# Performance work log

Hardware: AMD Instinct MI355X
Metric: run time of the kernel (lower is better)

## Reference

```python
import jax, jax.numpy as jnp
import numpy as np

B, L, D_MODEL = 4, 2048, 1024
D_STATE, D_CONV, EXPAND = 16, 4, 2
D_INNER = EXPAND * D_MODEL
DT_RANK = D_MODEL // 16
EPS = 1e-5


def layernorm(x, g, b):
    mu = jnp.mean(x, axis=-1, keepdims=True)
    var = jnp.mean(jnp.square(x - mu), axis=-1, keepdims=True)
    return (x - mu) * jax.lax.rsqrt(var + EPS) * g + b


def mamba(h, in_proj_w, conv_w, conv_b, x_proj_w, dt_proj_w, dt_proj_b, A_log, Dp, out_proj_w):
    # in projection -> [B, L, 2*D_INNER]
    xz = jnp.einsum('bld,ed->ble', h, in_proj_w)
    xi, z = jnp.split(xz, 2, axis=-1)
    # causal depthwise conv over time: [B, D_INNER, L]
    xc = jnp.transpose(xi, (0, 2, 1))
    xc = jax.lax.conv_general_dilated(
        xc, conv_w, window_strides=(1,), padding=[(D_CONV - 1, 0)],
        dimension_numbers=('NCH', 'OIH', 'NCH'), feature_group_count=D_INNER)
    xc = xc + conv_b[None, :, None]
    xi = jax.nn.silu(jnp.transpose(xc, (0, 2, 1)))  # [B, L, D_INNER]
    # data-dependent SSM params
    x_dbl = jnp.einsum('bld,ed->ble', xi, x_proj_w)  # [B, L, DT_RANK + 2*N]
    dt, Bm, Cm = jnp.split(x_dbl, [DT_RANK, DT_RANK + D_STATE], axis=-1)
    dt = jax.nn.softplus(jnp.einsum('blr,dr->bld', dt, dt_proj_w) + dt_proj_b)  # [B, L, D_INNER]
    A = -jnp.exp(A_log)  # [D_INNER, D_STATE]

    def step(hstate, inp):
        dt_t, B_t, C_t, u_t = inp  # [B,Din], [B,N], [B,N], [B,Din]
        dA = jnp.exp(dt_t[..., None] * A)                   # [B, Din, N]
        dBu = dt_t[..., None] * B_t[:, None, :] * u_t[..., None]
        hstate = dA * hstate + dBu
        y_t = jnp.sum(hstate * C_t[:, None, :], axis=-1)    # [B, Din]
        return hstate, y_t

    h0 = jnp.zeros((B, D_INNER, D_STATE), dtype=h.dtype)
    xs = (jnp.swapaxes(dt, 0, 1), jnp.swapaxes(Bm, 0, 1),
          jnp.swapaxes(Cm, 0, 1), jnp.swapaxes(xi, 0, 1))
    _, ys = jax.lax.scan(step, h0, xs)  # ys: [L, B, D_INNER]
    y = jnp.swapaxes(ys, 0, 1) + Dp * xi
    y = y * jax.nn.silu(z)
    return jnp.einsum('ble,de->bld', y, out_proj_w)


def setup_inputs() -> dict:
    key = jax.random.key(0)
    ks = jax.random.split(key, 16)
    s = 0.02
    inp = {
        'x': jax.random.normal(ks[0], (B, L, D_MODEL), jnp.float32),
        'ln1_g': jnp.ones((D_MODEL,), jnp.float32),
        'ln1_b': jnp.zeros((D_MODEL,), jnp.float32),
        'ln2_g': jnp.ones((D_MODEL,), jnp.float32),
        'ln2_b': jnp.zeros((D_MODEL,), jnp.float32),
        'in_proj_w': jax.random.normal(ks[1], (2 * D_INNER, D_MODEL), jnp.float32) * s,
        'conv_w': jax.random.normal(ks[2], (D_INNER, 1, D_CONV), jnp.float32) * 0.1,
        'conv_b': jnp.zeros((D_INNER,), jnp.float32),
        'x_proj_w': jax.random.normal(ks[3], (DT_RANK + 2 * D_STATE, D_INNER), jnp.float32) * s,
        'dt_proj_w': jax.random.normal(ks[4], (D_INNER, DT_RANK), jnp.float32) * 0.1,
        'dt_proj_b': jnp.full((D_INNER,), -4.0, jnp.float32),
        'A_log': jnp.log(jnp.broadcast_to(jnp.arange(1, D_STATE + 1, dtype=jnp.float32), (D_INNER, D_STATE))),
        'Dp': jnp.ones((D_INNER,), jnp.float32),
        'out_proj_w': jax.random.normal(ks[5], (D_MODEL, D_INNER), jnp.float32) * s,
        'ffn_w1': jax.random.normal(ks[6], (4 * D_MODEL, D_MODEL), jnp.float32) * s,
        'ffn_b1': jnp.zeros((4 * D_MODEL,), jnp.float32),
        'ffn_w2': jax.random.normal(ks[7], (D_MODEL, 4 * D_MODEL), jnp.float32) * s,
        'ffn_b2': jnp.zeros((D_MODEL,), jnp.float32),
    }
    return inp


def reference(x, ln1_g, ln1_b, ln2_g, ln2_b, in_proj_w, conv_w, conv_b, x_proj_w,
              dt_proj_w, dt_proj_b, A_log, Dp, out_proj_w, ffn_w1, ffn_b1, ffn_w2, ffn_b2):
    x = x + mamba(layernorm(x, ln1_g, ln1_b), in_proj_w, conv_w, conv_b,
                  x_proj_w, dt_proj_w, dt_proj_b, A_log, Dp, out_proj_w)
    h2 = layernorm(x, ln2_g, ln2_b)
    ffn = jnp.einsum('bld,fd->blf', h2, ffn_w1) + ffn_b1
    ffn = jnp.einsum('blf,df->bld', jax.nn.relu(ffn), ffn_w2) + ffn_b2
    return x + ffn  # dropout is identity in eval mode
```

## Files before the change

kernel.cpp:

```cpp
#include <hip/hip_runtime.h>

using u16 = unsigned short;
using u32 = unsigned int;

typedef short s16x8 __attribute__((ext_vector_type(8)));
typedef float f32x4 __attribute__((ext_vector_type(4)));

#define DEV static __device__ __forceinline__
#define AS1 __attribute__((address_space(1)))
#define AS3 __attribute__((address_space(3)))

DEV u16 f2bf(float f){
  u32 u = __float_as_uint(f);
  return (u16)((u + 0x7fffu + ((u >> 16) & 1u)) >> 16);
}
DEV float bf2f(u16 h){ return __uint_as_float(((u32)h) << 16); }

DEV void gload_lds16(const u16* g, u16* l){
  __builtin_amdgcn_global_load_lds((const AS1 void*)g, (AS3 void*)l, 16, 0, 0);
}

__global__ __launch_bounds__(256) void cast_w(
    const float* __restrict__ s0, const float* __restrict__ s1,
    const float* __restrict__ s2, const float* __restrict__ s3,
    const float* __restrict__ s4, const float* __restrict__ s5,
    u16* __restrict__ dst)
{
  size_t base = ((size_t)blockIdx.x * 256 + threadIdx.x) * 4;
  if (base >= 15007744u) return;
  const float* src; size_t off;
  if      (base <  4194304u){ src=s0; off=base;           }
  else if (base <  4390912u){ src=s1; off=base- 4194304u; }
  else if (base <  4521984u){ src=s2; off=base- 4390912u; }
  else if (base <  6619136u){ src=s3; off=base- 4521984u; }
  else if (base < 10813440u){ src=s4; off=base- 6619136u; }
  else                      { src=s5; off=base-10813440u; }
  float4 v = *(const float4*)(src + off);
  *(ushort4*)(dst + base) = make_ushort4(f2bf(v.x), f2bf(v.y), f2bf(v.z), f2bf(v.w));
}

__global__ __launch_bounds__(256) void ln_bf16(
    const float* __restrict__ x, const float* __restrict__ g,
    const float* __restrict__ b, u16* __restrict__ o)
{
  int row = blockIdx.x, t = threadIdx.x;
  float4 v = ((const float4*)(x + (size_t)row*1024))[t];
  float s  = v.x+v.y+v.z+v.w;
  float ss = v.x*v.x+v.y*v.y+v.z*v.z+v.w*v.w;
  #pragma unroll
  for (int off=32; off; off>>=1){ s += __shfl_down(s,off); ss += __shfl_down(ss,off); }
  __shared__ float red[8];
  int lane = t & 63, w = t >> 6;
  if (lane==0){ red[w]=s; red[4+w]=ss; }
  __syncthreads();
  float S  = red[0]+red[1]+red[2]+red[3];
  float SS = red[4]+red[5]+red[6]+red[7];
  float mu = S * (1.f/1024.f);
  float var = SS * (1.f/1024.f) - mu*mu;
  float rs = rsqrtf(var + 1e-5f);
  float4 gg = ((const float4*)g)[t], bb = ((const float4*)b)[t];
  ((ushort4*)o)[(size_t)row*256 + t] = make_ushort4(
    f2bf((v.x-mu)*rs*gg.x + bb.x), f2bf((v.y-mu)*rs*gg.y + bb.y),
    f2bf((v.z-mu)*rs*gg.z + bb.z), f2bf((v.w-mu)*rs*gg.w + bb.w));
}

__global__ __launch_bounds__(256) void conv_silu(
    const u16* __restrict__ xi, const float* __restrict__ cw,
    const float* __restrict__ cb, u16* __restrict__ ob)
{
  int idx = blockIdx.x*256 + threadIdx.x;
  int d4 = (idx & 511) << 2;
  int l  = (idx >> 9) & 2047;
  int b  = idx >> 20;
  float4 w0 = ((const float4*)cw)[d4+0];
  float4 w1 = ((const float4*)cw)[d4+1];
  float4 w2 = ((const float4*)cw)[d4+2];
  float4 w3 = ((const float4*)cw)[d4+3];
  float4 bb = *(const float4*)(cb + d4);
  float a0=bb.x, a1=bb.y, a2=bb.z, a3=bb.w;
  size_t rowbase = ((size_t)b*2048 + l)*2048 + d4;
  #pragma unroll
  for (int j=0;j<4;j++){
    int ls = l - 3 + j;
    if (ls >= 0){
      ushort4 xv = *(const ushort4*)(xi + rowbase + (size_t)(j-3)*2048);
      a0 += (&w0.x)[j]*bf2f(xv.x);
      a1 += (&w1.x)[j]*bf2f(xv.y);
      a2 += (&w2.x)[j]*bf2f(xv.z);
      a3 += (&w3.x)[j]*bf2f(xv.w);
    }
  }
  ushort4 o;
  o.x = f2bf(a0/(1.f+__expf(-a0)));
  o.y = f2bf(a1/(1.f+__expf(-a1)));
  o.z = f2bf(a2/(1.f+__expf(-a2)));
  o.w = f2bf(a3/(1.f+__expf(-a3)));
  *(ushort4*)(ob + rowbase) = o;
}

__global__ __launch_bounds__(256) void xred(
    const float* __restrict__ xp, float* __restrict__ xd, u16* __restrict__ dr)
{
  int i = blockIdx.x*256 + threadIdx.x;
  float v = xp[i] + xp[786432 + i] + xp[2*786432 + i] + xp[3*786432 + i];
  xd[i] = v;
  int row = i / 96, col = i - row*96;
  if (col < 64) dr[(size_t)row*64 + col] = f2bf(v);
}


__global__ __launch_bounds__(256) void scan_a(
    const u16* __restrict__ dtq, const u16* __restrict__ u,
    const float* __restrict__ xdbl, const float* __restrict__ alog,
    float* __restrict__ hend, float* __restrict__ sdt)
{
  int d = blockIdx.x*256 + threadIdx.x;
  int b = blockIdx.y, s = blockIdx.z, l0 = s*64;
  __shared__ float sB[64][16];
  for (int i = threadIdx.x; i < 1024; i += 256){
    int row = i >> 4, c = i & 15;
    sB[row][c] = xdbl[((size_t)(b*2048 + l0 + row))*96 + 64 + c];
  }
  float afn[16];
  #pragma unroll
  for (int n=0;n<16;n++) afn[n] = -__expf(alog[d*16+n]);
  __syncthreads();
  float h[16];
  #pragma unroll
  for (int n=0;n<16;n++) h[n] = 0.f;
  float sum_dt = 0.f;
  size_t base = ((size_t)b*2048 + l0)*2048 + d;
  for (int t=0;t<64;t++){
    float dtv = bf2f(dtq[base]);
    float uv  = bf2f(u[base]);
    sum_dt += dtv;
    float dtu = dtv*uv;
    #pragma unroll
    for (int n=0;n<16;n++)
      h[n] = __expf(dtv*afn[n])*h[n] + dtu*sB[t][n];
    base += 2048;
  }
  sdt[(b*32+s)*2048 + d] = sum_dt;
  size_t hb = ((size_t)(b*32+s)*16)*2048 + d;
  #pragma unroll
  for (int n=0;n<16;n++) hend[hb + (size_t)n*2048] = h[n];
}

__global__ __launch_bounds__(256) void scan_b(
    float* __restrict__ hend, const float* __restrict__ sdt,
    const float* __restrict__ alog)
{
  int g = blockIdx.x*256 + threadIdx.x;
  int d = g & 2047, n = (g >> 11) & 15, b = g >> 15;
  float An = -__expf(alog[d*16+n]);
  float h = 0.f;
  for (int s=0;s<32;s++){
    size_t hi = ((size_t)((b*32+s)*16) + n)*2048 + d;
    float he = hend[hi];
    hend[hi] = h;
    h = he + h*__expf(An * sdt[(b*32+s)*2048 + d]);
  }
}

__global__ __launch_bounds__(256) void scan_c(
    const u16* __restrict__ dtq, const u16* __restrict__ u,
    const u16* __restrict__ zb, const float* __restrict__ xdbl,
    const float* __restrict__ alog, const float* __restrict__ dp,
    const float* __restrict__ hstart, u16* __restrict__ yg)
{
  int d = blockIdx.x*256 + threadIdx.x;
  int b = blockIdx.y, s = blockIdx.z, l0 = s*64;
  __shared__ float sB[64][16], sC[64][16];
  for (int i = threadIdx.x; i < 1024; i += 256){
    int row = i >> 4, c = i & 15;
    size_t xb = ((size_t)(b*2048 + l0 + row))*96 + 64;
    sB[row][c] = xdbl[xb + c];
    sC[row][c] = xdbl[xb + 16 + c];
  }
  float afn[16];
  #pragma unroll
  for (int n=0;n<16;n++) afn[n] = -__expf(alog[d*16+n]);
  __syncthreads();
  float h[16];
  size_t hb = ((size_t)((b*32+s)*16))*2048 + d;
  #pragma unroll
  for (int n=0;n<16;n++) h[n] = hstart[hb + (size_t)n*2048];
  float Dpd = dp[d];
  size_t base = ((size_t)b*2048 + l0)*2048 + d;
  for (int t=0;t<64;t++){
    float dtv = bf2f(dtq[base]);
    float uv  = bf2f(u[base]);
    float dtu = dtv*uv;
    float y = 0.f;
    #pragma unroll
    for (int n=0;n<16;n++){
      h[n] = __expf(dtv*afn[n])*h[n] + dtu*sB[t][n];
      y += h[n]*sC[t][n];
    }
    float zv = bf2f(zb[base]);
    float yv = (y + Dpd*uv) * (zv / (1.f + __expf(-zv)));
    yg[base] = f2bf(yv);
    base += 2048;
  }
}

template<int EPI>
__global__ __launch_bounds__(256) void gemm_bt(
    const u16* __restrict__ A, const u16* __restrict__ W,
    int M, int N, int K, int Nreal,
    float* __restrict__ F0, const float* __restrict__ C0,
    const float* __restrict__ C1, u16* __restrict__ OB, u16* __restrict__ OB2)
{
  __shared__ __attribute__((aligned(16))) u16 sA[128*32];
  __shared__ __attribute__((aligned(16))) u16 sB[128*32];
  const int tid  = threadIdx.x;
  const int lane = tid & 63;
  const int wid  = tid >> 6;
  const int wr = wid >> 1, wc = wid & 1;
  const int bm = blockIdx.y * 128, bn = blockIdx.x * 128;

  const int kchunk = K / (int)gridDim.z;
  const int k0 = (int)blockIdx.z * kchunk, k1 = k0 + kchunk;

  f32x4 acc[4][4];
  #pragma unroll
  for (int m=0;m<4;m++)
    #pragma unroll
    for (int nn=0;nn<4;nn++) acc[m][nn] = (f32x4){0.f,0.f,0.f,0.f};

  const int c0 = tid,        r0a = c0 >> 2, cc0 = c0 & 3;
  const int c1 = tid + 256,  r1a = c1 >> 2, cc1 = c1 & 3;
  int wrow0 = bn + r0a; if (wrow0 > Nreal-1) wrow0 = Nreal-1;
  int wrow1 = bn + r1a; if (wrow1 > Nreal-1) wrow1 = Nreal-1;

  const int frow = lane & 15;
  const int ksel = lane >> 4;

  for (int kt = k0; kt < k1; kt += 32){
    gload_lds16(A + (size_t)(bm + r0a)*K + kt + cc0*8, &sA[c0*8]);
    gload_lds16(A + (size_t)(bm + r1a)*K + kt + cc1*8, &sA[c1*8]);
    gload_lds16(W + (size_t)wrow0*K + kt + cc0*8, &sB[c0*8]);
    gload_lds16(W + (size_t)wrow1*K + kt + cc1*8, &sB[c1*8]);
    __syncthreads();
    s16x8 af[4], bfr[4];
    #pragma unroll
    for (int m=0;m<4;m++)
      af[m] = *(const s16x8*)&sA[(wr*64 + m*16 + frow)*32 + ksel*8];
    #pragma unroll
    for (int nn=0;nn<4;nn++)
      bfr[nn] = *(const s16x8*)&sB[(wc*64 + nn*16 + frow)*32 + ksel*8];
    #pragma unroll
    for (int m=0;m<4;m++)
      #pragma unroll
      for (int nn=0;nn<4;nn++)
        acc[m][nn] = __builtin_amdgcn_mfma_f32_16x16x32_bf16(af[m], bfr[nn], acc[m][nn], 0, 0, 0);
    __syncthreads();
  }

  const int crow0 = (lane >> 4) * 4;
  const int ccol  = lane & 15;
  #pragma unroll
  for (int m=0;m<4;m++){
    #pragma unroll
    for (int nn=0;nn<4;nn++){
      #pragma unroll
      for (int j=0;j<4;j++){
        int grow = bm + wr*64 + m*16 + crow0 + j;
        int gcol = bn + wc*64 + nn*16 + ccol;
        float v = acc[m][nn][j];
        if constexpr (EPI==0){
          if (gcol < 2048) OB2[(size_t)grow*2048 + gcol] = f2bf(v);
          else             OB[(size_t)grow*2048 + (gcol-2048)] = f2bf(v);
        } else if constexpr (EPI==1){
          if (gcol < Nreal)
            F0[((size_t)blockIdx.z*M + grow)*Nreal + gcol] = v;
        } else if constexpr (EPI==2){
          v += C0[gcol];
          v = (v > 20.f) ? v : log1pf(__expf(v));
          OB[(size_t)grow*N + gcol] = f2bf(v);
        } else if constexpr (EPI==3){
          F0[(size_t)grow*N + gcol] = v + C1[(size_t)grow*N + gcol];
        } else if constexpr (EPI==4){
          v += C0[gcol]; v = fmaxf(v, 0.f);
          OB[(size_t)grow*N + gcol] = f2bf(v);
        } else {
          F0[(size_t)grow*N + gcol] = v + C0[gcol] + C1[(size_t)grow*N + gcol];
        }
      }
    }
  }
}

extern "C" void kernel_launch(void* const* d_in, const int* in_sizes, int n_in,
                              void* d_out, int out_size, void* d_ws, size_t ws_size,
                              hipStream_t stream)
{
  const float* X    = (const float*)d_in[0];
  const float* LN1G = (const float*)d_in[1];
  const float* LN1B = (const float*)d_in[2];
  const float* LN2G = (const float*)d_in[3];
  const float* LN2B = (const float*)d_in[4];
  const float* INW  = (const float*)d_in[5];
  const float* CONVW= (const float*)d_in[6];
  const float* CONVB= (const float*)d_in[7];
  const float* XPW  = (const float*)d_in[8];
  const float* DTW  = (const float*)d_in[9];
  const float* DTBIA= (const float*)d_in[10];
  const float* ALOG = (const float*)d_in[11];
  const float* DP   = (const float*)d_in[12];
  const float* OUTW = (const float*)d_in[13];
  const float* W1   = (const float*)d_in[14];
  const float* B1   = (const float*)d_in[15];
  const float* W2   = (const float*)d_in[16];
  const float* B2   = (const float*)d_in[17];

  char* ws = (char*)d_ws;
  u16* WB   = (u16*)ws;
  u16* bIN  = WB;
  u16* bXP  = WB + 4194304;
  u16* bDT  = WB + 4390912;
  u16* bOUT = WB + 4521984;
  u16* bW1  = WB + 6619136;
  u16* bW2  = WB + 10813440;
  u16*   H1    = (u16*)(ws + 30015488);
  float* HEND  = (float*)(ws + 30015488);
  u16*   ZB    = (u16*)(ws + 46792704);
  u16*   XIPRE = (u16*)(ws + 80347136);
  u16*   YG    = XIPRE;
  u16*   XIB   = (u16*)(ws + 113901568);
  u16*   DTQ   = (u16*)(ws + 147456000);
  float* XPART = (float*)(ws + 181010432);
  float* XDBL  = (float*)(ws + 193593344);
  u16*   DTRAW = (u16*)(ws + 196739072);
  float* SDT   = (float*)(ws + 196739072);
  u16*   F1    = ZB;
  float* X2    = (float*)d_out;

  cast_w<<<14656, 256, 0, stream>>>(INW, XPW, DTW, OUTW, W1, W2, WB);
  ln_bf16<<<8192, 256, 0, stream>>>(X, LN1G, LN1B, H1);
  gemm_bt<0><<<dim3(32,64,1), 256, 0, stream>>>(H1, bIN, 8192, 4096, 1024, 4096,
                                                nullptr, nullptr, nullptr, ZB, XIPRE);
  conv_silu<<<16384, 256, 0, stream>>>(XIPRE, CONVW, CONVB, XIB);
  gemm_bt<1><<<dim3(1,64,4), 256, 0, stream>>>(XIB, bXP, 8192, 128, 2048, 96,
                                               XPART, nullptr, nullptr, nullptr, nullptr);
  xred<<<3072, 256, 0, stream>>>(XPART, XDBL, DTRAW);
  gemm_bt<2><<<dim3(16,64,1), 256, 0, stream>>>(DTRAW, bDT, 8192, 2048, 64, 2048,
                                                nullptr, DTBIA, nullptr, DTQ, nullptr);
  scan_a<<<dim3(8,4,32), 256, 0, stream>>>(DTQ, XIB, XDBL, ALOG, HEND, SDT);
  scan_b<<<512, 256, 0, stream>>>(HEND, SDT, ALOG);
  scan_c<<<dim3(8,4,32), 256, 0, stream>>>(DTQ, XIB, ZB, XDBL, ALOG, DP, HEND, YG);
  gemm_bt<3><<<dim3(8,64,1), 256, 0, stream>>>(YG, bOUT, 8192, 1024, 2048, 1024,
                                               X2, nullptr, X, nullptr, nullptr);
  ln_bf16<<<8192, 256, 0, stream>>>(X2, LN2G, LN2B, H1);
  gemm_bt<4><<<dim3(32,64,1), 256, 0, stream>>>(H1, bW1, 8192, 4096, 1024, 4096,
                                                nullptr, B1, nullptr, F1, nullptr);
  gemm_bt<5><<<dim3(8,64,1), 256, 0, stream>>>(F1, bW2, 8192, 1024, 4096, 1024,
                                               (float*)d_out, B2, X2, nullptr, nullptr);
}
```

Before: 799.8 us.

## Add 256x256 double-buffered GEMM for wide projections and swizzle block order

Introduces a new 512-thread GEMM kernel with 256x256 output tiles, K-step 64, and double-buffered LDS staging through direct global-to-LDS loads. It is used for the in-projection and FFN-up GEMMs, aiming for more data reuse per tile and overlap of loads with MFMA work. All GEMMs also get a block-index swizzle that spreads consecutive workgroups across eight groups, intended to improve cache locality across XCDs. In exchange, register pressure from 32 accumulators per thread and 128KB of LDS per block may limit occupancy, and the unpadded LDS layout may cause bank conflicts.

```diff
diff --git a/kernel.cpp b/kernel.cpp
--- a/kernel.cpp
+++ b/kernel.cpp
@@ -108,7 +108,6 @@
   if (col < 64) dr[(size_t)row*64 + col] = f2bf(v);
 }
 
-
 __global__ __launch_bounds__(256) void scan_a(
     const u16* __restrict__ dtq, const u16* __restrict__ u,
     const float* __restrict__ xdbl, const float* __restrict__ alog,
@@ -204,6 +203,106 @@
   }
 }
 
+DEV void stage256(const u16* __restrict__ A, const u16* __restrict__ W,
+                  int K, int bm, int bn, int kt,
+                  u16* sA, u16* sB, int w, int lane)
+{
+  int rlo = lane >> 3, c8 = (lane & 7) * 8;
+  #pragma unroll
+  for (int j=0;j<4;j++){
+    int chunk = w*4 + j;
+    int row = chunk*8 + rlo;
+    gload_lds16(A + (size_t)(bm+row)*K + kt + c8, sA + chunk*512 + lane*8);
+    gload_lds16(W + (size_t)(bn+row)*K + kt + c8, sB + chunk*512 + lane*8);
+  }
+}
+
+template<int EPI>
+__global__ __launch_bounds__(512,2) void gemm256(
+    const u16* __restrict__ A, const u16* __restrict__ W,
+    int M, int N, int K,
+    const float* __restrict__ C0, u16* __restrict__ OB, u16* __restrict__ OB2)
+{
+  __shared__ __attribute__((aligned(16))) u16 sA[2][256*64];
+  __shared__ __attribute__((aligned(16))) u16 sB[2][256*64];
+  const int tid = threadIdx.x, lane = tid & 63, w = tid >> 6;
+  const int wr = w >> 2, wc = w & 3;
+  const int nbx = N >> 8;
+  const int nwg = (int)gridDim.x;
+  const int cpx = nwg >> 3;
+  const int bid = (int)blockIdx.x;
+  const int swz = (bid & 7)*cpx + (bid >> 3);
+  const int bm = (swz / nbx) * 256, bn = (swz % nbx) * 256;
+
+  f32x4 acc[8][4];
+  #pragma unroll
+  for (int m=0;m<8;m++)
+    #pragma unroll
+    for (int n=0;n<4;n++) acc[m][n] = (f32x4){0.f,0.f,0.f,0.f};
+
+  const int NT = K >> 6;
+  stage256(A, W, K, bm, bn, 0, sA[0], sB[0], w, lane);
+  __syncthreads();
+  int cur = 0;
+  const int frow = lane & 15, ksel = lane >> 4;
+  for (int t=0; t<NT; ++t){
+    if (t+1 < NT)
+      stage256(A, W, K, bm, bn, (t+1)<<6, sA[cur^1], sB[cur^1], w, lane);
+    const u16* a_ = sA[cur];
+    const u16* b_ = sB[cur];
+    #pragma unroll
+    for (int qm=0;qm<2;qm++){
+      s16x8 af[4][2];
+      #pragma unroll
+      for (int m=0;m<4;m++)
+        #pragma unroll
+        for (int ks=0;ks<2;ks++)
+          af[m][ks] = *(const s16x8*)&a_[(wr*128 + qm*64 + m*16 + frow)*64 + ks*32 + ksel*8];
+      #pragma unroll
+      for (int qn=0;qn<2;qn++){
+        s16x8 bfr[2][2];
+        #pragma unroll
+        for (int n2=0;n2<2;n2++)
+          #pragma unroll
+          for (int ks=0;ks<2;ks++)
+            bfr[n2][ks] = *(const s16x8*)&b_[(wc*64 + qn*32 + n2*16 + frow)*64 + ks*32 + ksel*8];
+        #pragma unroll
+        for (int m=0;m<4;m++)
+          #pragma unroll
+          for (int n2=0;n2<2;n2++)
+            #pragma unroll
+            for (int ks=0;ks<2;ks++)
+              acc[qm*4+m][qn*2+n2] = __builtin_amdgcn_mfma_f32_16x16x32_bf16(
+                  af[m][ks], bfr[n2][ks], acc[qm*4+m][qn*2+n2], 0, 0, 0);
+      }
+    }
+    __syncthreads();
+    cur ^= 1;
+  }
+
+  const int crow0 = (lane >> 4) * 4;
+  const int ccol  = lane & 15;
+  #pragma unroll
+  for (int mi=0;mi<8;mi++){
+    #pragma unroll
+    for (int ni=0;ni<4;ni++){
+      #pragma unroll
+      for (int j=0;j<4;j++){
+        int grow = bm + wr*128 + mi*16 + crow0 + j;
+        int gcol = bn + wc*64 + ni*16 + ccol;
+        float v = acc[mi][ni][j];
+        if constexpr (EPI==0){
+          if (gcol < 2048) OB2[(size_t)grow*2048 + gcol] = f2bf(v);
+          else             OB[(size_t)grow*2048 + (gcol-2048)] = f2bf(v);
+        } else {
+          v += C0[gcol]; v = fmaxf(v, 0.f);
+          OB[(size_t)grow*N + gcol] = f2bf(v);
+        }
+      }
+    }
+  }
+}
+
 template<int EPI>
 __global__ __launch_bounds__(256) void gemm_bt(
     const u16* __restrict__ A, const u16* __restrict__ W,
@@ -217,7 +316,12 @@
   const int lane = tid & 63;
   const int wid  = tid >> 6;
   const int wr = wid >> 1, wc = wid & 1;
-  const int bm = blockIdx.y * 128, bn = blockIdx.x * 128;
+  const int nbx = (int)gridDim.x;
+  const int nwg = nbx * (int)gridDim.y;
+  const int cpx = nwg >> 3;
+  const int bid = (int)blockIdx.y * nbx + (int)blockIdx.x;
+  const int swz = (bid & 7)*cpx + (bid >> 3);
+  const int bm = (swz / nbx) * 128, bn = (swz % nbx) * 128;
 
   const int kchunk = K / (int)gridDim.z;
   const int k0 = (int)blockIdx.z * kchunk, k1 = k0 + kchunk;
@@ -338,8 +442,8 @@
 
   cast_w<<<14656, 256, 0, stream>>>(INW, XPW, DTW, OUTW, W1, W2, WB);
   ln_bf16<<<8192, 256, 0, stream>>>(X, LN1G, LN1B, H1);
-  gemm_bt<0><<<dim3(32,64,1), 256, 0, stream>>>(H1, bIN, 8192, 4096, 1024, 4096,
-                                                nullptr, nullptr, nullptr, ZB, XIPRE);
+  gemm256<0><<<512, 512, 0, stream>>>(H1, bIN, 8192, 4096, 1024,
+                                      nullptr, ZB, XIPRE);
   conv_silu<<<16384, 256, 0, stream>>>(XIPRE, CONVW, CONVB, XIB);
   gemm_bt<1><<<dim3(1,64,4), 256, 0, stream>>>(XIB, bXP, 8192, 128, 2048, 96,
                                                XPART, nullptr, nullptr, nullptr, nullptr);
@@ -352,8 +456,8 @@
   gemm_bt<3><<<dim3(8,64,1), 256, 0, stream>>>(YG, bOUT, 8192, 1024, 2048, 1024,
                                                X2, nullptr, X, nullptr, nullptr);
   ln_bf16<<<8192, 256, 0, stream>>>(X2, LN2G, LN2B, H1);
-  gemm_bt<4><<<dim3(32,64,1), 256, 0, stream>>>(H1, bW1, 8192, 4096, 1024, 4096,
-                                                nullptr, B1, nullptr, F1, nullptr);
+  gemm256<4><<<512, 512, 0, stream>>>(H1, bW1, 8192, 4096, 1024,
+                                      B1, F1, nullptr);
   gemm_bt<5><<<dim3(8,64,1), 256, 0, stream>>>(F1, bW2, 8192, 1024, 4096, 1024,
                                                (float*)d_out, B2, X2, nullptr, nullptr);
 }
```

Result: no change. 786.9 us (-1.6%).
